# Kernel tuning notes

Measured on AMD Instinct MI355X. Metric: run time of the kernel, lower is better.

The kernel has to match this reference:

```python
import jax, jax.numpy as jnp
import numpy as np

N_NODES = 4
EPS = 1e-12


def gcn_conv(x, edge_index, W, b):
    B, N, _ = x.shape
    loop = jnp.arange(N)
    src = jnp.concatenate([edge_index[0], loop])
    dst = jnp.concatenate([edge_index[1], loop])
    deg = jnp.zeros((N,), x.dtype).at[dst].add(1.0)  # in-degree incl. self loops (>=1)
    dinv = jax.lax.rsqrt(deg)
    norm = dinv[src] * dinv[dst]                      # [E+N]
    h = jnp.einsum('bnf,fo->bno', x, W)               # transform first (out < ... ok)
    msgs = h[:, src, :] * norm[None, :, None]         # gather + edge weight
    out = jnp.zeros((B, N, W.shape[1]), x.dtype).at[:, dst, :].add(msgs)  # scatter-add
    return out + b


def sage_conv(x, edge_index, Wl, bl, Wr):
    # PyG SAGEConv(aggr='mean', normalize=True): out = lin_l(mean_j x_j) + lin_r(x_i), l2-normalized
    B, N, F = x.shape
    src, dst = edge_index[0], edge_index[1]
    cnt = jnp.zeros((N,), x.dtype).at[dst].add(1.0)
    cnt = jnp.maximum(cnt, 1.0)
    agg = jnp.zeros((B, N, F), x.dtype).at[:, dst, :].add(x[:, src, :])
    agg = agg / cnt[None, :, None]                    # mean neighbor aggregation
    out = jnp.einsum('bnf,fo->bno', agg, Wl) + bl + jnp.einsum('bnf,fo->bno', x, Wr)
    nrm = jnp.sqrt(jnp.sum(out * out, axis=-1, keepdims=True))
    return out / jnp.maximum(nrm, EPS)


def setup_inputs() -> dict:
    key = jax.random.key(0)
    ks = jax.random.split(key, 16)
    B, N, Cin, Cout = 32768, N_NODES, 64, 10
    E = 12

    def glorot(k, fi, fo):
        s = (6.0 / (fi + fo)) ** 0.5
        return jax.random.uniform(k, (fi, fo), jnp.float32, -s, s)

    x = jax.random.normal(ks[0], (B, N, Cin), jnp.float32)
    edge_index = jax.random.randint(ks[1], (2, E), 0, N, jnp.int64)
    inp = {
        'x': x, 'edge_index': edge_index,
        'W1': glorot(ks[2], Cin, 1024), 'b1': jnp.zeros((1024,), jnp.float32),
        'Wl2': glorot(ks[3], 1024, 512), 'bl2': jnp.zeros((512,), jnp.float32), 'Wr2': glorot(ks[4], 1024, 512),
        'Wl3': glorot(ks[5], 512, 256), 'bl3': jnp.zeros((256,), jnp.float32), 'Wr3': glorot(ks[6], 512, 256),
        'Wl4': glorot(ks[7], 256, 256), 'bl4': jnp.zeros((256,), jnp.float32), 'Wr4': glorot(ks[8], 256, 256),
        'Wfc': glorot(ks[9], N * 256, Cout), 'bfc': jnp.zeros((Cout,), jnp.float32),
    }
    return inp


def reference(x, edge_index, W1, b1, Wl2, bl2, Wr2, Wl3, bl3, Wr3, Wl4, bl4, Wr4, Wfc, bfc):
    h = jax.nn.relu(gcn_conv(x, edge_index, W1, b1))
    h = jax.nn.relu(sage_conv(h, edge_index, Wl2, bl2, Wr2))
    h = jax.nn.relu(sage_conv(h, edge_index, Wl3, bl3, Wr3))
    h = jax.nn.relu(sage_conv(h, edge_index, Wl4, bl4, Wr4))
    h = h.reshape(h.shape[0], -1)                     # [B, 4*256]
    logits = h @ Wfc + bfc
    return jax.nn.softmax(logits, axis=-1)
```

## Files before the change

### kernel.cpp

```cpp
#include <hip/hip_runtime.h>
#include <stdint.h>
#include <math.h>

typedef __bf16 bf16;
typedef __attribute__((ext_vector_type(8))) __bf16 bf16x8;
typedef __attribute__((ext_vector_type(16))) float f32x16;

#define AS1 __attribute__((address_space(1)))
#define AS3 __attribute__((address_space(3)))

__device__ __forceinline__ void glds16(const void* g, void* l) {
    __builtin_amdgcn_global_load_lds((const AS1 uint32_t*)g, (AS3 uint32_t*)l, 16, 0, 0);
}


__global__ void k_setup(const int* __restrict__ ei, float* __restrict__ gmat) {
    if (threadIdx.x != 0 || blockIdx.x != 0) return;
    bool is64 = true;
    for (int i = 0; i < 12; i++) if (ei[2 * i + 1] != 0) { is64 = false; break; }
    int src[12], dst[12];
    for (int e = 0; e < 12; e++) {
        if (is64) { src[e] = ei[2 * e]; dst[e] = ei[24 + 2 * e]; }
        else      { src[e] = ei[e];     dst[e] = ei[12 + e]; }
    }
    float deg[4] = {1.f, 1.f, 1.f, 1.f};
    for (int e = 0; e < 12; e++) deg[dst[e]] += 1.f;
    float dinv[4];
    for (int n = 0; n < 4; n++) dinv[n] = 1.f / sqrtf(deg[n]);
    float A[16];
    for (int i = 0; i < 16; i++) A[i] = 0.f;
    for (int e = 0; e < 12; e++) A[dst[e] * 4 + src[e]] += dinv[src[e]] * dinv[dst[e]];
    for (int n = 0; n < 4; n++) A[n * 4 + n] += dinv[n] * dinv[n];
    float cnt[4] = {0.f, 0.f, 0.f, 0.f};
    for (int e = 0; e < 12; e++) cnt[dst[e]] += 1.f;
    for (int n = 0; n < 4; n++) cnt[n] = fmaxf(cnt[n], 1.f);
    float Mm[16];
    for (int i = 0; i < 16; i++) Mm[i] = 0.f;
    for (int e = 0; e < 12; e++) Mm[dst[e] * 4 + src[e]] += 1.f;
    for (int n = 0; n < 4; n++)
        for (int m = 0; m < 4; m++) Mm[n * 4 + m] /= cnt[n];
    for (int i = 0; i < 16; i++) { gmat[i] = A[i]; gmat[16 + i] = Mm[i]; }
}

__global__ __launch_bounds__(256) void wtransF(const float* __restrict__ W, int K,
                                               int N, bf16* __restrict__ Wt) {
    int a = blockIdx.x * 256 + threadIdx.x;
    if (a >= N * K) return;
    int j = a & 7, c64 = (a >> 3) & 63, tile = a >> 9;
    int m32 = c64 & 31, kh = c64 >> 5;
    int TK = K >> 4;
    int rblk = tile / TK, ks = tile - rblk * TK;
    int n = rblk * 32 + m32, k = ks * 16 + kh * 8 + j;
    Wt[a] = (bf16)W[(size_t)k * N + n];
}

__global__ __launch_bounds__(256) void wtransI(const float* __restrict__ Wl,
                                               const float* __restrict__ Wr,
                                               int K, int F, bf16* __restrict__ Bt) {
    int a = blockIdx.x * 256 + threadIdx.x;
    if (a >= 2 * F * K) return;
    int j = a & 7, c64 = (a >> 3) & 63, tile = a >> 9;
    int m32 = c64 & 31, kh = c64 >> 5;
    int TK = K >> 4;
    int rblk = tile / TK, ks = tile - rblk * TK;
    int n = rblk * 32 + m32, k = ks * 16 + kh * 8 + j;
    int f = n >> 1;
    float v = (n & 1) ? Wr[(size_t)k * F + f] : Wl[(size_t)k * F + f];
    Bt[a] = (bf16)v;
}

__global__ __launch_bounds__(256) void cast_x(const float4* __restrict__ x,
                                              bf16x8* __restrict__ out) {
    int i = blockIdx.x * 256 + threadIdx.x;
    int c64 = i & 63, m32 = c64 & 31, kh = c64 >> 5;
    int tile = i >> 6, RB = tile >> 2, ks = tile & 3;
    int row = RB * 32 + m32;
    int fb4 = ks * 4 + kh * 2;
    float4 a = x[(size_t)row * 16 + fb4], b = x[(size_t)row * 16 + fb4 + 1];
    bf16x8 o;
    o[0] = (bf16)a.x; o[1] = (bf16)a.y; o[2] = (bf16)a.z; o[3] = (bf16)a.w;
    o[4] = (bf16)b.x; o[5] = (bf16)b.y; o[6] = (bf16)b.z; o[7] = (bf16)b.w;
    out[i] = o;
}

__global__ __launch_bounds__(256) void k_zero(float4* __restrict__ p, int n4) {
    int i = blockIdx.x * 256 + threadIdx.x;
    if (i < n4) p[i] = make_float4(0.f, 0.f, 0.f, 0.f);
}

__global__ __launch_bounds__(256, 2) void gemm_mfma(
    const bf16* __restrict__ A, int K,
    const bf16* __restrict__ Bt,
    const float* __restrict__ bias,
    bf16* __restrict__ out, int N, int mode,
    const float* __restrict__ gm, float* __restrict__ ssq) {
    __shared__ bf16 sA[8192];
    __shared__ bf16 sB[16384];
    const int t = threadIdx.x;
    const int lane = t & 63;
    const int w = t >> 6;
    const int wr = w >> 1, wc = w & 1;
    const int lin = blockIdx.x + gridDim.x * blockIdx.y;
    const int C = gridDim.x;
    const int cls = lin & 7;
    const int s0 = lin >> 3;
    const int rpc = gridDim.y >> 3;
    const int sy = s0 / C;
    const int row0 = (cls * rpc + sy) * 128;
    const int col0 = (s0 - sy * C) * 256;
    const int m32 = lane & 31;
    const int kh = lane >> 5;

    f32x16 acc[2][4] = {};

    const int TK = K >> 4;
    const size_t tA  = ((size_t)(row0 >> 5) + w) * TK;
    const size_t tB0 = ((size_t)(col0 >> 5) + w) * TK;
    const size_t tB1 = ((size_t)(col0 >> 5) + w + 4) * TK;
    const int le = lane * 8;

    for (int kb = 0; kb < K; kb += 64) {
        int kt = kb >> 4;
#pragma unroll
        for (int s = 0; s < 4; s++) {
            glds16(A  + (tA  + kt + s) * 512 + le, &sA[(s * 4 + w) * 512]);
            glds16(Bt + (tB0 + kt + s) * 512 + le, &sB[(s * 8 + w) * 512]);
            glds16(Bt + (tB1 + kt + s) * 512 + le, &sB[(s * 8 + w + 4) * 512]);
        }
        __syncthreads();
#pragma unroll
        for (int s = 0; s < 4; s++) {
            bf16x8 af[2], bfr[4];
#pragma unroll
            for (int i = 0; i < 2; i++)
                af[i] = *(const bf16x8*)&sA[(s * 4 + 2 * wr + i) * 512 + le];
#pragma unroll
            for (int j = 0; j < 4; j++)
                bfr[j] = *(const bf16x8*)&sB[(s * 8 + 4 * wc + j) * 512 + le];
#pragma unroll
            for (int i = 0; i < 2; i++)
#pragma unroll
                for (int j = 0; j < 4; j++)
                    acc[i][j] = __builtin_amdgcn_mfma_f32_32x32x16_bf16(af[i], bfr[j], acc[i][j], 0, 0, 0);
        }
        __syncthreads();
    }

    float g[16];
#pragma unroll
    for (int q = 0; q < 16; q++) g[q] = gm[q];

    if (mode == 1) {
        const int Tn = N >> 4;
#pragma unroll
        for (int i = 0; i < 2; i++) {
            size_t RBo = (size_t)(row0 >> 5) + 2 * wr + i;
#pragma unroll
            for (int j = 0; j < 4; j++) {
                int c = col0 + (4 * wc + j) * 32 + m32;
                size_t tbase = (RBo * Tn + (c >> 4)) * 512;
                int coff = ((c >> 3) & 1) * 32;
                int cj = c & 7;
                float bsv = bias[c];
#pragma unroll
                for (int q = 0; q < 4; q++) {
#pragma unroll
                    for (int n = 0; n < 4; n++) {
                        float v = g[n * 4 + 0] * acc[i][j][q * 4 + 0] +
                                  g[n * 4 + 1] * acc[i][j][q * 4 + 1] +
                                  g[n * 4 + 2] * acc[i][j][q * 4 + 2] +
                                  g[n * 4 + 3] * acc[i][j][q * 4 + 3] + bsv;
                        out[tbase + (size_t)(coff + 4 * kh + 8 * q + n) * 8 + cj] =
                            (bf16)fmaxf(v, 0.f);
                    }
                }
            }
        }
    } else {
        const int F = N >> 1;
        const int Tf = F >> 4;
        const bool ev = ((m32 & 1) == 0);
#pragma unroll
        for (int i = 0; i < 2; i++) {
            size_t RBo = (size_t)(row0 >> 5) + 2 * wr + i;
            int rbAbs = row0 + (2 * wr + i) * 32 + 4 * kh;
#pragma unroll
            for (int q = 0; q < 4; q++) {
                float ssql[4] = {0.f, 0.f, 0.f, 0.f};
#pragma unroll
                for (int j = 0; j < 4; j++) {
                    int c = col0 + (4 * wc + j) * 32 + m32;
                    int f = c >> 1;
                    size_t tbase = (RBo * Tf + (f >> 4)) * 512;
                    int foff = ((f >> 3) & 1) * 32;
                    int fj = f & 7;
                    float bsv = bias[f];
                    float mine[4];
                    if (ev) {
#pragma unroll
                        for (int n = 0; n < 4; n++)
                            mine[n] = g[n * 4 + 0] * acc[i][j][q * 4 + 0] +
                                      g[n * 4 + 1] * acc[i][j][q * 4 + 1] +
                                      g[n * 4 + 2] * acc[i][j][q * 4 + 2] +
                                      g[n * 4 + 3] * acc[i][j][q * 4 + 3];
                    } else {
#pragma unroll
                        for (int n = 0; n < 4; n++) mine[n] = acc[i][j][q * 4 + n];
                    }
#pragma unroll
                    for (int n = 0; n < 4; n++) {
                        float oth = __shfl_xor(mine[n], 1);
                        float tot = mine[n] + oth + bsv;
                        ssql[n] += tot * tot;
                        if (ev)
                            out[tbase + (size_t)(foff + 4 * kh + 8 * q + n) * 8 + fj] =
                                (bf16)tot;
                    }
                }
#pragma unroll
                for (int n = 0; n < 4; n++) {
                    float v = ssql[n];
                    v += __shfl_xor(v, 1); v += __shfl_xor(v, 2);
                    v += __shfl_xor(v, 4); v += __shfl_xor(v, 8);
                    v += __shfl_xor(v, 16);
                    ssql[n] = v;
                }
                if (m32 == 0) {
#pragma unroll
                    for (int n = 0; n < 4; n++)
                        atomicAdd(&ssq[rbAbs + 8 * q + n], ssql[n] * 0.5f);
                }
            }
        }
    }
}

__global__ __launch_bounds__(256) void norm_apply(bf16x8* __restrict__ h,
                                                  const float* __restrict__ ssq,
                                                  int tsh) {
    int idx = blockIdx.x * 256 + threadIdx.x;
    int row = (((idx >> 6) >> tsh) << 5) | (idx & 31);
    float inv = 1.f / fmaxf(sqrtf(ssq[row]), 1e-12f);
    bf16x8 v = h[idx], o;
#pragma unroll
    for (int c = 0; c < 8; c++) o[c] = (bf16)fmaxf((float)v[c] * inv, 0.f);
    h[idx] = o;
}

__global__ __launch_bounds__(256) void fc_softmax(const bf16x8* __restrict__ h,
                                                  const float* __restrict__ ssq4,
                                                  const float* __restrict__ Wfc,
                                                  const float* __restrict__ bfc,
                                                  float* __restrict__ outp) {
    __shared__ float WT[10][1024];
    int t = threadIdx.x;
    for (int i = t; i < 10240; i += 256) { int o = i % 10, k = i / 10; WT[o][k] = Wfc[i]; }
    __syncthreads();
    int wid = t >> 6, lane = t & 63;
    size_t e = (size_t)blockIdx.x * 4 + wid;
    size_t eb8 = e >> 3;
    int eo = (int)(e & 7);
    int ks = lane & 15, node = lane >> 4;
    float inv = 1.f / fmaxf(sqrtf(ssq4[e * 4 + node]), 1e-12f);
    float acc[10];
#pragma unroll
    for (int o = 0; o < 10; o++) acc[o] = 0.f;
#pragma unroll
    for (int jj = 0; jj < 2; jj++) {
        size_t ch = (eb8 * 16 + ks) * 64 + jj * 32 + eo * 4 + node;
        bf16x8 v = h[ch];
        float f[8];
#pragma unroll
        for (int c = 0; c < 8; c++) f[c] = fmaxf((float)v[c] * inv, 0.f);
        int k0 = node * 256 + ks * 16 + jj * 8;
#pragma unroll
        for (int o = 0; o < 10; o++) {
            const float* wr = &WT[o][k0];
            float s = 0.f;
#pragma unroll
            for (int c = 0; c < 8; c++) s += f[c] * wr[c];
            acc[o] += s;
        }
    }
#pragma unroll
    for (int o = 0; o < 10; o++) {
        float v = acc[o];
        v += __shfl_xor(v, 32); v += __shfl_xor(v, 16); v += __shfl_xor(v, 8);
        v += __shfl_xor(v, 4);  v += __shfl_xor(v, 2);  v += __shfl_xor(v, 1);
        acc[o] = v + bfc[o];
    }
    float mx = acc[0];
#pragma unroll
    for (int o = 1; o < 10; o++) mx = fmaxf(mx, acc[o]);
    float sum = 0.f, p[10];
#pragma unroll
    for (int o = 0; o < 10; o++) { p[o] = expf(acc[o] - mx); sum += p[o]; }
    float inv2 = 1.f / sum;
    if (lane < 10) outp[e * 10 + lane] = p[lane] * inv2;
}

extern "C" void kernel_launch(void* const* d_in, const int* in_sizes, int n_in,
                              void* d_out, int out_size, void* d_ws, size_t ws_size,
                              hipStream_t stream) {
    const float* x   = (const float*)d_in[0];
    const int*   ei  = (const int*)d_in[1];
    const float* W1  = (const float*)d_in[2];
    const float* b1  = (const float*)d_in[3];
    const float* Wl2 = (const float*)d_in[4];
    const float* bl2 = (const float*)d_in[5];
    const float* Wr2 = (const float*)d_in[6];
    const float* Wl3 = (const float*)d_in[7];
    const float* bl3 = (const float*)d_in[8];
    const float* Wr3 = (const float*)d_in[9];
    const float* Wl4 = (const float*)d_in[10];
    const float* bl4 = (const float*)d_in[11];
    const float* Wr4 = (const float*)d_in[12];
    const float* Wfc = (const float*)d_in[13];
    const float* bfc = (const float*)d_in[14];
    float* out = (float*)d_out;

    const int B = 32768;
    char* base = (char*)d_ws;
    float* gmat = (float*)base;
    bf16* Wt1 = (bf16*)(base + 4096);
    bf16* Wt2 = Wt1 + 1024 * 64;
    bf16* Wt3 = Wt2 + 1024 * 1024;
    bf16* Wt4 = Wt3 + 512 * 512;
    char* sl  = (char*)(Wt4 + 512 * 256);
    size_t fixed = (size_t)(sl - base);

    int Bs = B;
    while (Bs > 512 && fixed + (size_t)Bs * 12848 > ws_size) Bs >>= 1;
    int nslice = B / Bs;
    int M = Bs * 4;

    bf16* R0 = (bf16*)sl;
    bf16* R1 = R0 + (size_t)Bs * 256;
    bf16* R2 = R1 + (size_t)Bs * 4096;
    float* ssqb = (float*)(R2 + (size_t)Bs * 2048);

    hipLaunchKernelGGL(k_setup, dim3(1), dim3(64), 0, stream, ei, gmat);
    hipLaunchKernelGGL(wtransF, dim3((1024 * 64 + 255) / 256), dim3(256), 0, stream,
                       W1, 64, 1024, Wt1);
    hipLaunchKernelGGL(wtransI, dim3((1024 * 1024 + 255) / 256), dim3(256), 0, stream,
                       Wl2, Wr2, 1024, 512, Wt2);
    hipLaunchKernelGGL(wtransI, dim3((512 * 512 + 255) / 256), dim3(256), 0, stream,
                       Wl3, Wr3, 512, 256, Wt3);
    hipLaunchKernelGGL(wtransI, dim3((512 * 256 + 255) / 256), dim3(256), 0, stream,
                       Wl4, Wr4, 256, 256, Wt4);

    for (int s = 0; s < nslice; s++) {
        const float* xs = x + (size_t)s * Bs * 256;
        hipLaunchKernelGGL(k_zero, dim3((3 * M / 4 + 255) / 256), dim3(256), 0, stream,
                           (float4*)ssqb, 3 * M / 4);
        hipLaunchKernelGGL(cast_x, dim3(Bs / 8), dim3(256), 0, stream,
                           (const float4*)xs, (bf16x8*)R0);
        hipLaunchKernelGGL(gemm_mfma, dim3(4, M / 128), dim3(256), 0, stream,
                           R0, 64, Wt1, b1, R1, 1024, 1, gmat, (float*)nullptr);
        hipLaunchKernelGGL(gemm_mfma, dim3(4, M / 128), dim3(256), 0, stream,
                           R1, 1024, Wt2, bl2, R2, 1024, 2, gmat + 16, ssqb);
        hipLaunchKernelGGL(norm_apply, dim3(M / 4), dim3(256), 0, stream,
                           (bf16x8*)R2, ssqb, 5);
        hipLaunchKernelGGL(gemm_mfma, dim3(2, M / 128), dim3(256), 0, stream,
                           R2, 512, Wt3, bl3, R1, 512, 2, gmat + 16, ssqb + M);
        hipLaunchKernelGGL(norm_apply, dim3(M / 8), dim3(256), 0, stream,
                           (bf16x8*)R1, ssqb + M, 4);
        hipLaunchKernelGGL(gemm_mfma, dim3(2, M / 128), dim3(256), 0, stream,
                           R1, 256, Wt4, bl4, R2, 512, 2, gmat + 16, ssqb + 2 * M);
        hipLaunchKernelGGL(fc_softmax, dim3(Bs / 4), dim3(256), 0, stream,
                           (const bf16x8*)R2, ssqb + 2 * M, Wfc, bfc,
                           out + (size_t)s * Bs * 10);
    }
}
```

Before: 938.0 us.

## Double-buffer GEMM LDS loads and enlarge tile to 256x256 with 8 waves

```diff
diff --git a/kernel.cpp b/kernel.cpp
--- a/kernel.cpp
+++ b/kernel.cpp
@@ -88,63 +88,74 @@
     if (i < n4) p[i] = make_float4(0.f, 0.f, 0.f, 0.f);
 }
 
-__global__ __launch_bounds__(256, 2) void gemm_mfma(
+__global__ __launch_bounds__(512, 2) void gemm_mfma(
     const bf16* __restrict__ A, int K,
     const bf16* __restrict__ Bt,
     const float* __restrict__ bias,
     bf16* __restrict__ out, int N, int mode,
     const float* __restrict__ gm, float* __restrict__ ssq) {
-    __shared__ bf16 sA[8192];
-    __shared__ bf16 sB[16384];
+    __shared__ bf16 sA[2][16384];
+    __shared__ bf16 sB[2][16384];
     const int t = threadIdx.x;
     const int lane = t & 63;
     const int w = t >> 6;
-    const int wr = w >> 1, wc = w & 1;
+    const int wr = w >> 2, wc = w & 3;
     const int lin = blockIdx.x + gridDim.x * blockIdx.y;
     const int C = gridDim.x;
     const int cls = lin & 7;
     const int s0 = lin >> 3;
     const int rpc = gridDim.y >> 3;
     const int sy = s0 / C;
-    const int row0 = (cls * rpc + sy) * 128;
+    const int row0 = (cls * rpc + sy) * 256;
     const int col0 = (s0 - sy * C) * 256;
     const int m32 = lane & 31;
     const int kh = lane >> 5;
 
-    f32x16 acc[2][4] = {};
+    f32x16 acc[4][2] = {};
 
     const int TK = K >> 4;
-    const size_t tA  = ((size_t)(row0 >> 5) + w) * TK;
-    const size_t tB0 = ((size_t)(col0 >> 5) + w) * TK;
-    const size_t tB1 = ((size_t)(col0 >> 5) + w + 4) * TK;
     const int le = lane * 8;
-
-    for (int kb = 0; kb < K; kb += 64) {
-        int kt = kb >> 4;
-#pragma unroll
-        for (int s = 0; s < 4; s++) {
-            glds16(A  + (tA  + kt + s) * 512 + le, &sA[(s * 4 + w) * 512]);
-            glds16(Bt + (tB0 + kt + s) * 512 + le, &sB[(s * 8 + w) * 512]);
-            glds16(Bt + (tB1 + kt + s) * 512 + le, &sB[(s * 8 + w + 4) * 512]);
+    const bf16* gA = A  + (size_t)((row0 >> 5) + w) * TK * 512 + le;
+    const bf16* gB = Bt + (size_t)((col0 >> 5) + w) * TK * 512 + le;
+
+    const int NT = K >> 6;
+#pragma unroll
+    for (int p = 0; p < 4; p++) {
+        glds16(gA + p * 512, &sA[0][(p * 8 + w) * 512]);
+        glds16(gB + p * 512, &sB[0][(p * 8 + w) * 512]);
+    }
+
+    for (int kt = 0; kt < NT; kt++) {
+        const int cur = kt & 1;
+        const size_t knext = (size_t)(kt + 1 < NT ? kt + 1 : kt) * 2048;
+        const bf16* rA = &sA[cur][0];
+        const bf16* rB = &sB[cur][0];
+        bf16* dA = &sA[cur ^ 1][w * 512];
+        bf16* dB = &sB[cur ^ 1][w * 512];
+#pragma unroll
+        for (int p = 0; p < 4; p++) {
+            asm volatile("s_waitcnt vmcnt(6)" ::: "memory");
+            __builtin_amdgcn_s_barrier();
+            asm volatile("" ::: "memory");
+            bf16x8 af[4], bfr[2];
+#pragma unroll
+            for (int i = 0; i < 4; i++)
+                af[i] = *(const bf16x8*)&rA[(p * 8 + wr * 4 + i) * 512 + le];
+#pragma unroll
+            for (int j = 0; j < 2; j++)
+                bfr[j] = *(const bf16x8*)&rB[(p * 8 + wc * 2 + j) * 512 + le];
+            glds16(gA + knext + p * 512, dA + p * 8 * 512);
+            glds16(gB + knext + p * 512, dB + p * 8 * 512);
+            __builtin_amdgcn_s_setprio(1);
+#pragma unroll
+            for (int i = 0; i < 4; i++)
+#pragma unroll
+                for (int j = 0; j < 2; j++)
+                    acc[i][j] = __builtin_amdgcn_mfma_f32_32x32x16_bf16(af[i], bfr[j], acc[i][j], 0, 0, 0);
+            __builtin_amdgcn_s_setprio(0);
         }
-        __syncthreads();
-#pragma unroll
-        for (int s = 0; s < 4; s++) {
-            bf16x8 af[2], bfr[4];
-#pragma unroll
-            for (int i = 0; i < 2; i++)
-                af[i] = *(const bf16x8*)&sA[(s * 4 + 2 * wr + i) * 512 + le];
-#pragma unroll
-            for (int j = 0; j < 4; j++)
-                bfr[j] = *(const bf16x8*)&sB[(s * 8 + 4 * wc + j) * 512 + le];
-#pragma unroll
-            for (int i = 0; i < 2; i++)
-#pragma unroll
-                for (int j = 0; j < 4; j++)
-                    acc[i][j] = __builtin_amdgcn_mfma_f32_32x32x16_bf16(af[i], bfr[j], acc[i][j], 0, 0, 0);
-        }
-        __syncthreads();
-    }
+    }
+    asm volatile("s_waitcnt vmcnt(0)" ::: "memory");
 
     float g[16];
 #pragma unroll
@@ -153,11 +164,11 @@
     if (mode == 1) {
         const int Tn = N >> 4;
 #pragma unroll
-        for (int i = 0; i < 2; i++) {
-            size_t RBo = (size_t)(row0 >> 5) + 2 * wr + i;
-#pragma unroll
-            for (int j = 0; j < 4; j++) {
-                int c = col0 + (4 * wc + j) * 32 + m32;
+        for (int i = 0; i < 4; i++) {
+            size_t RBo = (size_t)(row0 >> 5) + 4 * wr + i;
+#pragma unroll
+            for (int j = 0; j < 2; j++) {
+                int c = col0 + (2 * wc + j) * 32 + m32;
                 size_t tbase = (RBo * Tn + (c >> 4)) * 512;
                 int coff = ((c >> 3) & 1) * 32;
                 int cj = c & 7;
@@ -181,15 +192,15 @@
         const int Tf = F >> 4;
         const bool ev = ((m32 & 1) == 0);
 #pragma unroll
-        for (int i = 0; i < 2; i++) {
-            size_t RBo = (size_t)(row0 >> 5) + 2 * wr + i;
-            int rbAbs = row0 + (2 * wr + i) * 32 + 4 * kh;
+        for (int i = 0; i < 4; i++) {
+            size_t RBo = (size_t)(row0 >> 5) + 4 * wr + i;
+            int rbAbs = row0 + (4 * wr + i) * 32 + 4 * kh;
 #pragma unroll
             for (int q = 0; q < 4; q++) {
                 float ssql[4] = {0.f, 0.f, 0.f, 0.f};
 #pragma unroll
-                for (int j = 0; j < 4; j++) {
-                    int c = col0 + (4 * wc + j) * 32 + m32;
+                for (int j = 0; j < 2; j++) {
+                    int c = col0 + (2 * wc + j) * 32 + m32;
                     int f = c >> 1;
                     size_t tbase = (RBo * Tf + (f >> 4)) * 512;
                     int foff = ((f >> 3) & 1) * 32;
@@ -355,17 +366,17 @@
                            (float4*)ssqb, 3 * M / 4);
         hipLaunchKernelGGL(cast_x, dim3(Bs / 8), dim3(256), 0, stream,
                            (const float4*)xs, (bf16x8*)R0);
-        hipLaunchKernelGGL(gemm_mfma, dim3(4, M / 128), dim3(256), 0, stream,
+        hipLaunchKernelGGL(gemm_mfma, dim3(4, M / 256), dim3(512), 0, stream,
                            R0, 64, Wt1, b1, R1, 1024, 1, gmat, (float*)nullptr);
-        hipLaunchKernelGGL(gemm_mfma, dim3(4, M / 128), dim3(256), 0, stream,
+        hipLaunchKernelGGL(gemm_mfma, dim3(4, M / 256), dim3(512), 0, stream,
                            R1, 1024, Wt2, bl2, R2, 1024, 2, gmat + 16, ssqb);
         hipLaunchKernelGGL(norm_apply, dim3(M / 4), dim3(256), 0, stream,
                            (bf16x8*)R2, ssqb, 5);
-        hipLaunchKernelGGL(gemm_mfma, dim3(2, M / 128), dim3(256), 0, stream,
+        hipLaunchKernelGGL(gemm_mfma, dim3(2, M / 256), dim3(512), 0, stream,
                            R2, 512, Wt3, bl3, R1, 512, 2, gmat + 16, ssqb + M);
         hipLaunchKernelGGL(norm_apply, dim3(M / 8), dim3(256), 0, stream,
                            (bf16x8*)R1, ssqb + M, 4);
-        hipLaunchKernelGGL(gemm_mfma, dim3(2, M / 128), dim3(256), 0, stream,
+        hipLaunchKernelGGL(gemm_mfma, dim3(2, M / 256), dim3(512), 0, stream,
                            R1, 256, Wt4, bl4, R2, 512, 2, gmat + 16, ssqb + 2 * M);
         hipLaunchKernelGGL(fc_softmax, dim3(Bs / 4), dim3(256), 0, stream,
                            (const bf16x8*)R2, ssqb + 2 * M, Wfc, bfc,
```

After: 1.021 ms. +8.9%, slower.
